# Kernel tuning notes

Measured on AMD Instinct MI355X. Metric: run time of the kernel, lower is better.

Reference implementation:

```python
import jax, jax.numpy as jnp
import numpy as np

B, S, D = 256, 128, 512  # batch, seq_len, in_dim == hidden_dim


def _xavier(key, shape):
    fan_in, fan_out = shape[0], shape[1]
    lim = float(np.sqrt(6.0 / (fan_in + fan_out)))
    return jax.random.uniform(key, shape, jnp.float32, -lim, lim)


def setup_inputs() -> dict:
    key = jax.random.key(0)
    ks = jax.random.split(key, 13)
    return {
        "x": jax.random.normal(ks[0], (B, S, D), jnp.float32),
        "item": jax.random.normal(ks[1], (B, D), jnp.float32),
        "h0": _xavier(ks[2], (B, D)),
        "Wu": _xavier(ks[3], (D, D)),
        "Uu": _xavier(ks[4], (D, D)),
        "bu": _xavier(ks[5], (1, D)),
        "Wr": _xavier(ks[6], (D, D)),
        "Ur": _xavier(ks[7], (D, D)),
        "br": _xavier(ks[8], (1, D)),
        "Wh": _xavier(ks[9], (D, D)),
        "Uh": _xavier(ks[10], (D, D)),
        "bh": _xavier(ks[11], (1, D)),
        "Wa": _xavier(ks[12], (D, D)),
    }


def reference(x, item, h0, Wu, Uu, bu, Wr, Ur, br, Wh, Uh, bh, Wa):
    def step(h, xt):  # h, xt: [B, D]
        u = jax.nn.sigmoid(xt @ Wu + h @ Uu + bu)
        r = jax.nn.sigmoid(xt @ Wr + h @ Ur + br)
        h_hat = jnp.tanh(xt @ Wh + r * (h @ Uh) + bh)
        # attention: softmax over a length-1 axis (faithful to original; equals 1)
        score = jnp.sum((xt @ Wa) * item, axis=1, keepdims=True)  # [B, 1]
        a = jax.nn.softmax(score, axis=1)
        u_hat = a * u
        h_new = (1.0 - u_hat) * h + u_hat * h_hat
        return h_new, h_new

    xs = jnp.swapaxes(x, 0, 1)  # [S, B, D]
    h_last, outs = jax.lax.scan(step, h0, xs)
    outs = jnp.swapaxes(outs, 0, 1)  # [B, S, D]
    return outs, h_last
```

## Files before the change

kernel.cpp:

```cpp
#include <hip/hip_runtime.h>

#define DD 512
#define BB 256
#define SS 128
#define MTOT (BB*SS)
#define GROUPS 8
#define WPG 32
#define NWG (GROUPS*WPG)
#define NTHR 256
#define SLOTS (SS+1)

typedef __bf16 bf16;
typedef float f32x4 __attribute__((ext_vector_type(4)));
typedef __bf16 bf16x8 __attribute__((ext_vector_type(8)));

__device__ __forceinline__ float sigm(float z){ return 1.f/(1.f+__expf(-z)); }
__device__ __forceinline__ unsigned short b2u(bf16 v){ union{bf16 b; unsigned short u;} x; x.b=v; return x.u; }

__global__ void k_zero(int* c, int n){ for (int i=threadIdx.x; i<n; i+=NTHR) c[i]=0; }

__global__ __launch_bounds__(256) void k_cvtx(const float* __restrict__ X, bf16* __restrict__ Xb){
  size_t total = (size_t)MTOT*DD;
  for (size_t i = ((size_t)blockIdx.x*256 + threadIdx.x)*8; i < total; i += (size_t)gridDim.x*256*8){
    float4 a = *(const float4*)(X+i), b = *(const float4*)(X+i+4);
    bf16x8 v;
    v[0]=(bf16)a.x; v[1]=(bf16)a.y; v[2]=(bf16)a.z; v[3]=(bf16)a.w;
    v[4]=(bf16)b.x; v[5]=(bf16)b.y; v[6]=(bf16)b.z; v[7]=(bf16)b.w;
    *(bf16x8*)(Xb+i) = v;
  }
}

__device__ __forceinline__ void swapG(unsigned* a, unsigned v){
  unsigned old;
  asm volatile("global_atomic_swap %0, %1, %2, off sc0 sc1" : "=v"(old) : "v"(a), "v"(v) : "memory");
}

#define LDH(I,J) asm volatile("global_load_dwordx4 %0, %1, off offset:" #J " sc0 sc1" : "=&v"(av[I]) : "v"(g))
#define LDX(I,J) asm volatile("global_load_dwordx4 %0, %1, off offset:" #J : "=&v"(av[I]) : "v"(g))

__launch_bounds__(NTHR, 1)
__global__ void k_main(const bf16* __restrict__ xb, const float* __restrict__ h0,
                       const float* __restrict__ Wu, const float* __restrict__ Uu, const float* __restrict__ bu,
                       const float* __restrict__ Wr, const float* __restrict__ Ur, const float* __restrict__ br,
                       const float* __restrict__ Wh, const float* __restrict__ Uh, const float* __restrict__ bh,
                       bf16* hb0, bf16* hb1,
                       int* cnt, float* __restrict__ out, float* __restrict__ hlast){
  extern __shared__ char smem[];
  float* Xch = (float*)smem;
  bf16*  Hn  = (bf16*)(smem + 8192);

  const int tid = threadIdx.x, w = tid>>6, lane = tid&63;
  const int grp = blockIdx.x & 7, widx = blockIdx.x >> 3;
  const int m0 = grp*32, d0 = widx*16;
  int* const cbase = cnt + grp*SLOTS;
  const int mf = w&1, half = w>>1;

  bf16x8 bfr[3][16];
  {
    const float* mats[3];
    if (half){ mats[0]=Wu; mats[1]=Wr; mats[2]=Wh; }
    else     { mats[0]=Uu; mats[1]=Ur; mats[2]=Uh; }
    const int col = d0 + (lane&15);
    const int kr0 = (lane>>4)*8;
    #pragma unroll
    for (int g=0; g<3; ++g){
      const float* M = mats[g] + col;
      #pragma unroll
      for (int kc=0; kc<16; ++kc){
        bf16x8 v;
        #pragma unroll
        for (int j=0;j<8;j++) v[j] = (bf16)M[(size_t)(kc*32 + kr0 + j)*DD];
        bfr[g][kc] = v;
      }
    }
  }
  const int dcol = d0 + (lane&15);
  const float bu_v = bu[dcol], br_v = br[dcol], bh_v = bh[dcol];
  float hp[4];
  if (w < 2){
    #pragma unroll
    for (int j=0;j<4;j++)
      hp[j] = h0[(size_t)(m0 + mf*16 + (lane>>4)*4 + j)*DD + dcol];
  }
  const int pm = tid>>3, pdc = tid&7;
  unsigned* const packdst0 = (unsigned*)(hb0 + (size_t)(m0+pm)*DD + d0 + pdc*2);
  unsigned* const packdst1 = (unsigned*)(hb1 + (size_t)(m0+pm)*DD + d0 + pdc*2);
  {
    const float* src = h0 + (size_t)(m0+pm)*DD + d0 + pdc*2;
    unsigned pv = (unsigned)b2u((bf16)src[0]) | ((unsigned)b2u((bf16)src[1]) << 16);
    swapG(packdst0, pv);
    asm volatile("s_waitcnt vmcnt(0)" ::: "memory");
  }
  __syncthreads();
  if (tid==0){
    unsigned old, v;
    asm volatile("global_atomic_add %0, %1, %2, off sc0 sc1" : "=v"(old) : "v"(cbase), "v"(1u) : "memory");
    do { __builtin_amdgcn_s_sleep(2);
         asm volatile("global_load_dword %0, %1, off sc0 sc1\n\ts_waitcnt vmcnt(0)" : "=v"(v) : "v"(cbase) : "memory");
    } while (v < WPG);
  }
  __syncthreads();

  const int arow = mf*16 + (lane&15);
  const int coff = lane>>4;
  const bf16* const hA0 = hb0 + (size_t)(m0+arow)*DD + coff*8;
  const bf16* const hA1 = hb1 + (size_t)(m0+arow)*DD + coff*8;
  const bf16* const xA  = xb + (size_t)(m0+arow)*SS*DD + coff*8;

  bf16x8 av[16];
  if (half){
    const bf16* g = xA;
    LDX(0,0); LDX(1,64); LDX(2,128); LDX(3,192); LDX(4,256); LDX(5,320); LDX(6,384); LDX(7,448);
    LDX(8,512); LDX(9,576); LDX(10,640); LDX(11,704); LDX(12,768); LDX(13,832); LDX(14,896); LDX(15,960);
  }

  for (int st=0; st<SS; st++){
    if (!half){
      const bf16* g = (st&1)? hA1 : hA0;
      LDH(0,0); LDH(1,64); LDH(2,128); LDH(3,192); LDH(4,256); LDH(5,320); LDH(6,384); LDH(7,448);
      LDH(8,512); LDH(9,576); LDH(10,640); LDH(11,704); LDH(12,768); LDH(13,832); LDH(14,896); LDH(15,960);
    }
    asm volatile("s_waitcnt vmcnt(0)" ::: "memory");
    __builtin_amdgcn_sched_barrier(0);
    f32x4 acc0{}, acc1{}, acc2{};
    #pragma unroll
    for (int it=0; it<16; it++){
      acc0 = __builtin_amdgcn_mfma_f32_16x16x32_bf16(av[it], bfr[0][it], acc0, 0,0,0);
      acc1 = __builtin_amdgcn_mfma_f32_16x16x32_bf16(av[it], bfr[1][it], acc1, 0,0,0);
      acc2 = __builtin_amdgcn_mfma_f32_16x16x32_bf16(av[it], bfr[2][it], acc2, 0,0,0);
    }
    if (half){
      float* dst = Xch + (size_t)(mf*64 + lane)*12;
      *(f32x4*)(dst+0) = acc0; *(f32x4*)(dst+4) = acc1; *(f32x4*)(dst+8) = acc2;
    }
    __syncthreads();
    f32x4 hnv{};
    if (!half){
      const float* src = Xch + (size_t)(mf*64 + lane)*12;
      f32x4 p0 = *(const f32x4*)(src+0);
      f32x4 p1 = *(const f32x4*)(src+4);
      f32x4 p2 = *(const f32x4*)(src+8);
      int mlocal = mf*16 + (lane>>4)*4;
      #pragma unroll
      for (int j=0;j<4;j++){
        float u  = sigm(acc0[j] + p0[j] + bu_v);
        float rr = sigm(acc1[j] + p1[j] + br_v);
        float hh = tanhf(p2[j] + bh_v + rr*acc2[j]);
        float hn = (1.f-u)*hp[j] + u*hh;
        hp[j] = hn;
        hnv[j] = hn;
        Hn[(mlocal+j)*20 + (lane&15)] = (bf16)hn;
      }
    } else if (st < SS-1){
      const bf16* g = xA + (size_t)(st+1)*DD;
      LDX(0,0); LDX(1,64); LDX(2,128); LDX(3,192); LDX(4,256); LDX(5,320); LDX(6,384); LDX(7,448);
      LDX(8,512); LDX(9,576); LDX(10,640); LDX(11,704); LDX(12,768); LDX(13,832); LDX(14,896); LDX(15,960);
    }
    __syncthreads();
    if (st < SS-1){
      unsigned pv = (unsigned)b2u(Hn[pm*20 + pdc*2]) | ((unsigned)b2u(Hn[pm*20 + pdc*2 + 1]) << 16);
      unsigned* pd = (st&1)? packdst0 : packdst1;
      swapG(pd, pv);
      asm volatile("s_waitcnt vmcnt(0)" ::: "memory");
      __syncthreads();
      if (tid==0){
        unsigned v;
        int* cp = cbase + st + 1;
        asm volatile("global_atomic_add %0, %1, off sc1" :: "v"(cp), "v"(1u) : "memory");
        do { __builtin_amdgcn_s_sleep(2);
             asm volatile("global_load_dword %0, %1, off sc0 sc1\n\ts_waitcnt vmcnt(0)" : "=v"(v) : "v"(cp) : "memory");
        } while (v < WPG);
      }
      __syncthreads();
    }
    if (!half){
      int mlocal = mf*16 + (lane>>4)*4;
      #pragma unroll
      for (int j=0;j<4;j++){
        int m = m0 + mlocal + j;
        out[((size_t)m*SS + st)*DD + dcol] = hnv[j];
        if (st == SS-1) hlast[(size_t)m*DD + dcol] = hnv[j];
      }
    }
  }
}

extern "C" void kernel_launch(void* const* d_in, const int* in_sizes, int n_in,
                              void* d_out, int out_size, void* d_ws, size_t ws_size,
                              hipStream_t stream){
  const float* x   = (const float*)d_in[0];
  const float* h0  = (const float*)d_in[2];
  const float* Wu  = (const float*)d_in[3];
  const float* Uu  = (const float*)d_in[4];
  const float* bu  = (const float*)d_in[5];
  const float* Wr  = (const float*)d_in[6];
  const float* Ur  = (const float*)d_in[7];
  const float* br  = (const float*)d_in[8];
  const float* Wh  = (const float*)d_in[9];
  const float* Uh  = (const float*)d_in[10];
  const float* bh  = (const float*)d_in[11];
  float* out   = (float*)d_out;
  float* hlast = out + (size_t)MTOT*DD;

  char* ws = (char*)d_ws;
  bf16* xb  = (bf16*)(ws);
  bf16* hb0 = (bf16*)(ws + 0x2000000);
  bf16* hb1 = (bf16*)(ws + 0x2040000);
  int*  cnt = (int*)(ws + 0x2080000);

  k_cvtx<<<dim3(2048), dim3(256), 0, stream>>>(x, xb);
  k_zero<<<dim3(1), dim3(NTHR), 0, stream>>>(cnt, GROUPS*SLOTS);
  k_main<<<dim3(NWG), dim3(NTHR), 16384, stream>>>(
      xb, h0, Wu, Uu, bu, Wr, Ur, br, Wh, Uh, bh, hb0, hb1, cnt, out, hlast);
}
```

Measured before the change: 546.9 us.

## Publish hidden state directly from compute waves via shuffles and per-wave counters

The two recurrent-compute waves now pack their new hidden values into bf16 pairs using lane shuffles and write them straight to the global exchange buffer. This removes the LDS staging buffer, one block barrier and the thread-0 handoff. Each compute wave increments the step counter itself and spins until it reaches twice the workgroup count, while the input-projection waves prefetch the next x tile in parallel. The gain is a shorter per-step critical path; the cost is twice as many atomic arrivals and pollers per counter, and shared memory is reduced to 8 KB.

Result: slower. 631.9 us (+15.6%).

```diff
diff --git a/kernel.cpp b/kernel.cpp
--- a/kernel.cpp
+++ b/kernel.cpp
@@ -47,7 +47,6 @@
                        int* cnt, float* __restrict__ out, float* __restrict__ hlast){
   extern __shared__ char smem[];
   float* Xch = (float*)smem;
-  bf16*  Hn  = (bf16*)(smem + 8192);
 
   const int tid = threadIdx.x, w = tid>>6, lane = tid&63;
   const int grp = blockIdx.x & 7, widx = blockIdx.x >> 3;
@@ -82,13 +81,12 @@
     for (int j=0;j<4;j++)
       hp[j] = h0[(size_t)(m0 + mf*16 + (lane>>4)*4 + j)*DD + dcol];
   }
-  const int pm = tid>>3, pdc = tid&7;
-  unsigned* const packdst0 = (unsigned*)(hb0 + (size_t)(m0+pm)*DD + d0 + pdc*2);
-  unsigned* const packdst1 = (unsigned*)(hb1 + (size_t)(m0+pm)*DD + d0 + pdc*2);
   {
+    const int pm = tid>>3, pdc = tid&7;
+    unsigned* pd = (unsigned*)(hb0 + (size_t)(m0+pm)*DD + d0 + pdc*2);
     const float* src = h0 + (size_t)(m0+pm)*DD + d0 + pdc*2;
     unsigned pv = (unsigned)b2u((bf16)src[0]) | ((unsigned)b2u((bf16)src[1]) << 16);
-    swapG(packdst0, pv);
+    swapG(pd, pv);
     asm volatile("s_waitcnt vmcnt(0)" ::: "memory");
   }
   __syncthreads();
@@ -106,6 +104,10 @@
   const bf16* const hA0 = hb0 + (size_t)(m0+arow)*DD + coff*8;
   const bf16* const hA1 = hb1 + (size_t)(m0+arow)*DD + coff*8;
   const bf16* const xA  = xb + (size_t)(m0+arow)*SS*DD + coff*8;
+  const int rowA = mf*16 + (lane>>4)*4 + ((lane&1)<<1);
+  const int cpair = d0 + ((lane&15)&14);
+  unsigned* const pubA0 = (unsigned*)(hb0 + (size_t)(m0+rowA)*DD + cpair);
+  unsigned* const pubA1 = (unsigned*)(hb1 + (size_t)(m0+rowA)*DD + cpair);
 
   bf16x8 av[16];
   if (half){
@@ -140,7 +142,6 @@
       f32x4 p0 = *(const f32x4*)(src+0);
       f32x4 p1 = *(const f32x4*)(src+4);
       f32x4 p2 = *(const f32x4*)(src+8);
-      int mlocal = mf*16 + (lane>>4)*4;
       #pragma unroll
       for (int j=0;j<4;j++){
         float u  = sigm(acc0[j] + p0[j] + bu_v);
@@ -149,27 +150,35 @@
         float hn = (1.f-u)*hp[j] + u*hh;
         hp[j] = hn;
         hnv[j] = hn;
-        Hn[(mlocal+j)*20 + (lane&15)] = (bf16)hn;
-      }
-    } else if (st < SS-1){
-      const bf16* g = xA + (size_t)(st+1)*DD;
-      LDX(0,0); LDX(1,64); LDX(2,128); LDX(3,192); LDX(4,256); LDX(5,320); LDX(6,384); LDX(7,448);
-      LDX(8,512); LDX(9,576); LDX(10,640); LDX(11,704); LDX(12,768); LDX(13,832); LDX(14,896); LDX(15,960);
-    }
-    __syncthreads();
+      }
+    }
     if (st < SS-1){
-      unsigned pv = (unsigned)b2u(Hn[pm*20 + pdc*2]) | ((unsigned)b2u(Hn[pm*20 + pdc*2 + 1]) << 16);
-      unsigned* pd = (st&1)? packdst0 : packdst1;
-      swapG(pd, pv);
-      asm volatile("s_waitcnt vmcnt(0)" ::: "memory");
-      __syncthreads();
-      if (tid==0){
+      if (!half){
+        float nb0 = __shfl_xor(hnv[0],1), nb1 = __shfl_xor(hnv[1],1);
+        float nb2 = __shfl_xor(hnv[2],1), nb3 = __shfl_xor(hnv[3],1);
+        unsigned vA, vB;
+        if (lane&1){
+          vA = (unsigned)b2u((bf16)nb2)     | ((unsigned)b2u((bf16)hnv[2])<<16);
+          vB = (unsigned)b2u((bf16)nb3)     | ((unsigned)b2u((bf16)hnv[3])<<16);
+        } else {
+          vA = (unsigned)b2u((bf16)hnv[0])  | ((unsigned)b2u((bf16)nb0)<<16);
+          vB = (unsigned)b2u((bf16)hnv[1])  | ((unsigned)b2u((bf16)nb1)<<16);
+        }
+        unsigned* pA = (st&1)? pubA0 : pubA1;
+        swapG(pA, vA);
+        swapG(pA + DD/2, vB);
+        asm volatile("s_waitcnt vmcnt(0)" ::: "memory");
+        int* cp = cbase + st + 1;
+        if (lane==0)
+          asm volatile("global_atomic_add %0, %1, off sc1" :: "v"(cp), "v"(1u) : "memory");
         unsigned v;
-        int* cp = cbase + st + 1;
-        asm volatile("global_atomic_add %0, %1, off sc1" :: "v"(cp), "v"(1u) : "memory");
         do { __builtin_amdgcn_s_sleep(2);
              asm volatile("global_load_dword %0, %1, off sc0 sc1\n\ts_waitcnt vmcnt(0)" : "=v"(v) : "v"(cp) : "memory");
-        } while (v < WPG);
+        } while (v < 2*WPG);
+      } else {
+        const bf16* g = xA + (size_t)(st+1)*DD;
+        LDX(0,0); LDX(1,64); LDX(2,128); LDX(3,192); LDX(4,256); LDX(5,320); LDX(6,384); LDX(7,448);
+        LDX(8,512); LDX(9,576); LDX(10,640); LDX(11,704); LDX(12,768); LDX(13,832); LDX(14,896); LDX(15,960);
       }
       __syncthreads();
     }
@@ -210,6 +219,6 @@
 
   k_cvtx<<<dim3(2048), dim3(256), 0, stream>>>(x, xb);
   k_zero<<<dim3(1), dim3(NTHR), 0, stream>>>(cnt, GROUPS*SLOTS);
-  k_main<<<dim3(NWG), dim3(NTHR), 16384, stream>>>(
+  k_main<<<dim3(NWG), dim3(NTHR), 8192, stream>>>(
       xb, h0, Wu, Uu, bu, Wr, Ur, br, Wh, Uh, bh, hb0, hb1, cnt, out, hlast);
 }
```
